# Kernel tuning notes

Measured on AMD Instinct MI355X. Metric: run time of the kernel, lower is better.

## Reference

```python
import jax, jax.numpy as jnp
import numpy as np

NUM_NODES = 100000
NUM_HYPEREDGES = 20000
NUM_SEMALINKS = 5000
NUM_EDGES = 600000
IN_DIM = 128
SIGNAL_DIM = 64
OUT_DIM = 128


def setup_inputs() -> dict:
    key = jax.random.key(0)
    k = jax.random.split(key, 8)
    node_embeddings = jax.random.normal(k[0], (NUM_NODES, IN_DIM), dtype=jnp.float32)
    semalink_embeddings = jax.random.normal(k[1], (NUM_SEMALINKS, SIGNAL_DIM), dtype=jnp.float32)
    hyperedge_embeddings = jax.random.normal(k[2], (NUM_HYPEREDGES, IN_DIM), dtype=jnp.float32)
    node_idx = jax.random.randint(k[3], (NUM_EDGES,), 0, NUM_NODES, dtype=jnp.int32)
    sl_idx = jax.random.randint(k[4], (NUM_EDGES,), 0, NUM_SEMALINKS, dtype=jnp.int32)
    he_idx = jax.random.randint(k[5], (NUM_EDGES,), 0, NUM_HYPEREDGES, dtype=jnp.int32)
    semalinks = jnp.stack([node_idx, sl_idx, he_idx], axis=1)  # [E, 3]
    W_a = jax.random.normal(k[6], (IN_DIM, SIGNAL_DIM), dtype=jnp.float32)
    W_f = jax.random.normal(k[7], (2 * IN_DIM, OUT_DIM), dtype=jnp.float32)
    return {
        'node_embeddings': node_embeddings,
        'semalink_embeddings': semalink_embeddings,
        'hyperedge_embeddings': hyperedge_embeddings,
        'semalinks': semalinks,
        'W_a': W_a,
        'W_f': W_f,
    }


def reference(node_embeddings, semalink_embeddings, hyperedge_embeddings, semalinks, W_a, W_f):
    # Original loops edges in order, ASSIGNING final_embeddings[node_idx] each time:
    # only the LAST edge touching each node determines that node's output.
    E = semalinks.shape[0]
    n_idx = semalinks[:, 0]
    s_idx = semalinks[:, 1]
    h_idx = semalinks[:, 2]

    order = jnp.arange(E, dtype=jnp.int32)
    last = jax.ops.segment_max(order, n_idx, num_segments=NUM_NODES)  # [N]
    has_edge = last >= 0
    last_c = jnp.clip(last, 0, E - 1)

    sel_h = h_idx[last_c]  # [N]
    sel_s = s_idx[last_c]  # [N]
    h_emb = hyperedge_embeddings[sel_h]          # [N, in_dim]
    sl_emb = semalink_embeddings[sel_s]          # [N, signal_dim]

    # per-node attention score (1x1 in original)
    r_h = node_embeddings @ W_a                  # [N, signal_dim]
    r_t = h_emb @ W_a                            # [N, signal_dim]
    score = jnp.sum(r_h * jnp.tanh(r_t + sl_emb), axis=-1, keepdims=True)  # [N, 1]
    gamma = jax.nn.softmax(score, axis=-1)       # softmax over singleton == 1.0 (same as torch)
    f = gamma * h_emb                            # [N, in_dim]

    u = jnp.concatenate([f, node_embeddings], axis=-1) @ W_f  # [N, out_dim]
    out = jnp.where(has_edge[:, None], u, jnp.zeros((), dtype=u.dtype))
    return out
```

## Files before the change

### kernel.cpp

```cpp
#include <hip/hip_runtime.h>
#include <hip/hip_bf16.h>

#define NNODES 100000
#define NHE 20000
#define NEDGES 600000

typedef float f32x4 __attribute__((ext_vector_type(4)));
typedef short bf16x8 __attribute__((ext_vector_type(8)));
typedef short bf16x4 __attribute__((ext_vector_type(4)));
typedef int i32x4 __attribute__((ext_vector_type(4)));
typedef unsigned long long u64;

__device__ __forceinline__ unsigned short f2bf(float f) {
    unsigned u = __builtin_bit_cast(unsigned, f);
    u += 0x7fffu + ((u >> 16) & 1u);
    return (unsigned short)(u >> 16);
}
__device__ __forceinline__ float bf2f(unsigned short h) {
    unsigned u = ((unsigned)h) << 16;
    return __builtin_bit_cast(float, u);
}

__global__ void k0(u64* __restrict__ packed, const float* __restrict__ Wf,
                   unsigned short* __restrict__ wt) {
    int b = blockIdx.x, t = threadIdx.x;
    if (b < 196) {
        int i = b * 256 + t;
        if (i < NNODES / 2) ((f32x4*)packed)[i] = (f32x4){0.f, 0.f, 0.f, 0.f};
    } else {
        int idx = (b - 196) * 256 + t;
        int k = idx >> 7, c = idx & 127;
        wt[c * 256 + k] = f2bf(Wf[idx]);
    }
}

__global__ __launch_bounds__(256) void k1(
    const int* __restrict__ sl, u64* __restrict__ packed,
    const float* __restrict__ he_emb, const unsigned short* __restrict__ wt,
    unsigned short* __restrict__ heo)
{
    int b = blockIdx.x, t = threadIdx.x;
    if (b < 586) {
        int tg = b * 256 + t;
        if (tg < NEDGES / 4) {
            const i32x4* s4 = (const i32x4*)sl;
            i32x4 a = s4[3 * tg], bb = s4[3 * tg + 1], c = s4[3 * tg + 2];
            int e0 = 4 * tg;
            atomicMax(&packed[a[0]], ((u64)(e0 + 1) << 32) | (unsigned)a[2]);
            atomicMax(&packed[a[3]], ((u64)(e0 + 2) << 32) | (unsigned)bb[1]);
            atomicMax(&packed[bb[2]], ((u64)(e0 + 3) << 32) | (unsigned)c[0]);
            atomicMax(&packed[c[1]], ((u64)(e0 + 4) << 32) | (unsigned)c[3]);
        }
        return;
    }

    __shared__ __align__(16) unsigned short Xs[64 * 128];
    int r0 = (b - 586) * 64;

    #pragma unroll
    for (int i = 0; i < 8; ++i) {
        int idx = i * 256 + t;
        int row = idx >> 5, q = idx & 31;
        int ri = r0 + row; if (ri >= NHE) ri = NHE - 1;
        f32x4 v = *(const f32x4*)(he_emb + (long)ri * 128 + q * 4);
        bf16x4 p;
        p[0] = (short)f2bf(v[0]); p[1] = (short)f2bf(v[1]);
        p[2] = (short)f2bf(v[2]); p[3] = (short)f2bf(v[3]);
        int byte = (row * 256 + q * 8) ^ ((row & 7) << 4);
        *(bf16x4*)((char*)Xs + byte) = p;
    }
    __syncthreads();

    int lane = t & 63, w = t >> 6;
    int wm = w >> 1, wn = w & 1;
    int l15 = lane & 15, l4 = lane >> 4;

    f32x4 acc[2][4] = {};
    #pragma unroll
    for (int kc = 0; kc < 2; ++kc)
        #pragma unroll
        for (int ks = 0; ks < 2; ++ks) {
            bf16x8 a[2], bb[4];
            #pragma unroll
            for (int fm = 0; fm < 2; ++fm) {
                int row = wm * 32 + fm * 16 + l15;
                int byte = (row * 256 + kc * 128 + ks * 64 + l4 * 16) ^ ((row & 7) << 4);
                a[fm] = *(const bf16x8*)((const char*)Xs + byte);
            }
            #pragma unroll
            for (int fn = 0; fn < 4; ++fn) {
                int col = wn * 64 + fn * 16 + l15;
                bb[fn] = *(const bf16x8*)(wt + (long)col * 256 + kc * 64 + ks * 32 + l4 * 8);
            }
            #pragma unroll
            for (int fm = 0; fm < 2; ++fm)
                #pragma unroll
                for (int fn = 0; fn < 4; ++fn)
                    acc[fm][fn] = __builtin_amdgcn_mfma_f32_16x16x32_bf16(
                        bb[fn], a[fm], acc[fm][fn], 0, 0, 0);
        }

    #pragma unroll
    for (int fm = 0; fm < 2; ++fm) {
        int ri = r0 + wm * 32 + fm * 16 + l15;
        if (ri < NHE) {
            #pragma unroll
            for (int fn = 0; fn < 4; ++fn) {
                bf16x4 p;
                p[0] = (short)f2bf(acc[fm][fn][0]);
                p[1] = (short)f2bf(acc[fm][fn][1]);
                p[2] = (short)f2bf(acc[fm][fn][2]);
                p[3] = (short)f2bf(acc[fm][fn][3]);
                *(bf16x4*)(heo + (long)ri * 128 + wn * 64 + fn * 16 + l4 * 4) = p;
            }
        }
    }
}

__global__ __launch_bounds__(256) void k_main(
    const float* __restrict__ node_emb,
    const u64* __restrict__ packed,
    const unsigned short* __restrict__ wt,
    const unsigned short* __restrict__ heo,
    float* __restrict__ out)
{
    __shared__ __align__(16) unsigned short Xs[64 * 128];

    int t = threadIdx.x;
    int r0 = blockIdx.x * 64;
    int lane = t & 63, w = t >> 6;
    int wm = w >> 1, wn = w & 1;
    int l15 = lane & 15, l4 = lane >> 4;

    u64 p = 0;
    {
        int prow = r0 + wm * 32 + (lane & 31);
        if (lane < 32 && prow < NNODES) p = packed[prow];
    }

    f32x4 nv[8];
    #pragma unroll
    for (int i = 0; i < 8; ++i) {
        int idx = i * 256 + t;
        int row = idx >> 5, q = idx & 31;
        int ri = r0 + row; if (ri >= NNODES) ri = NNODES - 1;
        nv[i] = *(const f32x4*)(node_emb + (long)ri * 128 + q * 4);
    }

    int he16 = (int)(p & 0xffffffffull);
    int v16 = (p != 0) ? 1 : 0;
    int hrow[2], vv[2];
    hrow[0] = __shfl(he16, l15, 64);       vv[0] = __shfl(v16, l15, 64);
    hrow[1] = __shfl(he16, 16 + l15, 64);  vv[1] = __shfl(v16, 16 + l15, 64);
    bf16x4 hv[2][4];
    #pragma unroll
    for (int fm = 0; fm < 2; ++fm)
        #pragma unroll
        for (int fn = 0; fn < 4; ++fn)
            hv[fm][fn] = *(const bf16x4*)(heo + (long)hrow[fm] * 128 +
                                          wn * 64 + fn * 16 + l4 * 4);

    #pragma unroll
    for (int i = 0; i < 8; ++i) {
        int idx = i * 256 + t;
        int row = idx >> 5, q = idx & 31;
        bf16x4 pk;
        pk[0] = (short)f2bf(nv[i][0]); pk[1] = (short)f2bf(nv[i][1]);
        pk[2] = (short)f2bf(nv[i][2]); pk[3] = (short)f2bf(nv[i][3]);
        int byte = (row * 256 + q * 8) ^ ((row & 7) << 4);
        *(bf16x4*)((char*)Xs + byte) = pk;
    }

    asm volatile("s_waitcnt lgkmcnt(0)" ::: "memory");
    __builtin_amdgcn_sched_barrier(0);
    __builtin_amdgcn_s_barrier();
    __builtin_amdgcn_sched_barrier(0);

    f32x4 acc[2][4] = {};
    #pragma unroll
    for (int kc = 0; kc < 2; ++kc)
        #pragma unroll
        for (int ks = 0; ks < 2; ++ks) {
            bf16x8 a[2], b[4];
            #pragma unroll
            for (int fm = 0; fm < 2; ++fm) {
                int row = wm * 32 + fm * 16 + l15;
                int byte = (row * 256 + kc * 128 + ks * 64 + l4 * 16) ^ ((row & 7) << 4);
                a[fm] = *(const bf16x8*)((const char*)Xs + byte);
            }
            #pragma unroll
            for (int fn = 0; fn < 4; ++fn) {
                int col = wn * 64 + fn * 16 + l15;
                b[fn] = *(const bf16x8*)(wt + (long)col * 256 + 128 + kc * 64 + ks * 32 + l4 * 8);
            }
            #pragma unroll
            for (int fm = 0; fm < 2; ++fm)
                #pragma unroll
                for (int fn = 0; fn < 4; ++fn)
                    acc[fm][fn] = __builtin_amdgcn_mfma_f32_16x16x32_bf16(
                        b[fn], a[fm], acc[fm][fn], 0, 0, 0);
        }

    #pragma unroll
    for (int fm = 0; fm < 2; ++fm) {
        int ri = r0 + wm * 32 + fm * 16 + l15;
        if (ri < NNODES) {
            int v = vv[fm];
            #pragma unroll
            for (int fn = 0; fn < 4; ++fn) {
                f32x4 o;
                #pragma unroll
                for (int jj = 0; jj < 4; ++jj)
                    o[jj] = v ? (acc[fm][fn][jj] + bf2f((unsigned short)hv[fm][fn][jj]))
                              : 0.0f;
                __builtin_nontemporal_store(o,
                    (f32x4*)(out + (long)ri * 128 + wn * 64 + fn * 16 + l4 * 4));
            }
        }
    }
}

extern "C" void kernel_launch(void* const* d_in, const int* in_sizes, int n_in,
                              void* d_out, int out_size, void* d_ws, size_t ws_size,
                              hipStream_t stream) {
    const float* node_emb = (const float*)d_in[0];
    const float* he_emb = (const float*)d_in[2];
    const int* sl = (const int*)d_in[3];
    const float* Wf = (const float*)d_in[5];
    float* out = (float*)d_out;

    u64* packed = (u64*)d_ws;
    unsigned short* wt = (unsigned short*)((char*)d_ws + 800000);
    unsigned short* heo = (unsigned short*)((char*)d_ws + 865536);

    k0<<<324, 256, 0, stream>>>(packed, Wf, wt);
    k1<<<586 + 313, 256, 0, stream>>>(sl, packed, he_emb, wt, heo);
    k_main<<<(NNODES + 63) / 64, 256, 0, stream>>>(node_emb, packed, wt, heo, out);
}
```

Before: 70.08 us.

## Process two 64-row tiles per block with prefetch of second tile

Each k_main block now handles 128 node rows as two 64-row tiles with separate LDS buffers. The node embeddings for the second tile are loaded while the first tile's MFMA runs, and the packed/hyperedge gathers for both tiles are issued up front. This is meant to hide global load latency and amortize weight fragment loads. In exchange it raises register and LDS use and halves the grid size, which may reduce occupancy and tail balance.

```diff
diff --git a/kernel.cpp b/kernel.cpp
--- a/kernel.cpp
+++ b/kernel.cpp
@@ -124,18 +124,18 @@
     const unsigned short* __restrict__ heo,
     float* __restrict__ out)
 {
-    __shared__ __align__(16) unsigned short Xs[64 * 128];
+    __shared__ __align__(16) unsigned short Xs[2][64 * 128];
 
     int t = threadIdx.x;
-    int r0 = blockIdx.x * 64;
+    int r0 = blockIdx.x * 128;
     int lane = t & 63, w = t >> 6;
     int wm = w >> 1, wn = w & 1;
     int l15 = lane & 15, l4 = lane >> 4;
 
     u64 p = 0;
     {
-        int prow = r0 + wm * 32 + (lane & 31);
-        if (lane < 32 && prow < NNODES) p = packed[prow];
+        int prow = r0 + (lane >> 5) * 64 + wm * 32 + (lane & 31);
+        if (prow < NNODES) p = packed[prow];
     }
 
     f32x4 nv[8];
@@ -149,16 +149,22 @@
 
     int he16 = (int)(p & 0xffffffffull);
     int v16 = (p != 0) ? 1 : 0;
-    int hrow[2], vv[2];
-    hrow[0] = __shfl(he16, l15, 64);       vv[0] = __shfl(v16, l15, 64);
-    hrow[1] = __shfl(he16, 16 + l15, 64);  vv[1] = __shfl(v16, 16 + l15, 64);
-    bf16x4 hv[2][4];
+    int hrow0[2], vv0[2], hrow1[2], vv1[2];
+    #pragma unroll
+    for (int fm = 0; fm < 2; ++fm) {
+        hrow0[fm] = __shfl(he16, fm * 16 + l15, 64);
+        vv0[fm]   = __shfl(v16,  fm * 16 + l15, 64);
+        hrow1[fm] = __shfl(he16, 32 + fm * 16 + l15, 64);
+        vv1[fm]   = __shfl(v16,  32 + fm * 16 + l15, 64);
+    }
+    bf16x4 hv0[2][4], hv1[2][4];
     #pragma unroll
     for (int fm = 0; fm < 2; ++fm)
         #pragma unroll
-        for (int fn = 0; fn < 4; ++fn)
-            hv[fm][fn] = *(const bf16x4*)(heo + (long)hrow[fm] * 128 +
-                                          wn * 64 + fn * 16 + l4 * 4);
+        for (int fn = 0; fn < 4; ++fn) {
+            hv0[fm][fn] = *(const bf16x4*)(heo + (long)hrow0[fm] * 128 + wn * 64 + fn * 16 + l4 * 4);
+            hv1[fm][fn] = *(const bf16x4*)(heo + (long)hrow1[fm] * 128 + wn * 64 + fn * 16 + l4 * 4);
+        }
 
     #pragma unroll
     for (int i = 0; i < 8; ++i) {
@@ -168,7 +174,7 @@
         pk[0] = (short)f2bf(nv[i][0]); pk[1] = (short)f2bf(nv[i][1]);
         pk[2] = (short)f2bf(nv[i][2]); pk[3] = (short)f2bf(nv[i][3]);
         int byte = (row * 256 + q * 8) ^ ((row & 7) << 4);
-        *(bf16x4*)((char*)Xs + byte) = pk;
+        *(bf16x4*)((char*)Xs[0] + byte) = pk;
     }
 
     asm volatile("s_waitcnt lgkmcnt(0)" ::: "memory");
@@ -176,6 +182,14 @@
     __builtin_amdgcn_s_barrier();
     __builtin_amdgcn_sched_barrier(0);
 
+    #pragma unroll
+    for (int i = 0; i < 8; ++i) {
+        int idx = i * 256 + t;
+        int row = idx >> 5, q = idx & 31;
+        int ri = r0 + 64 + row; if (ri >= NNODES) ri = NNODES - 1;
+        nv[i] = *(const f32x4*)(node_emb + (long)ri * 128 + q * 4);
+    }
+
     f32x4 acc[2][4] = {};
     #pragma unroll
     for (int kc = 0; kc < 2; ++kc)
@@ -186,7 +200,7 @@
             for (int fm = 0; fm < 2; ++fm) {
                 int row = wm * 32 + fm * 16 + l15;
                 int byte = (row * 256 + kc * 128 + ks * 64 + l4 * 16) ^ ((row & 7) << 4);
-                a[fm] = *(const bf16x8*)((const char*)Xs + byte);
+                a[fm] = *(const bf16x8*)((const char*)Xs[0] + byte);
             }
             #pragma unroll
             for (int fn = 0; fn < 4; ++fn) {
@@ -205,14 +219,71 @@
     for (int fm = 0; fm < 2; ++fm) {
         int ri = r0 + wm * 32 + fm * 16 + l15;
         if (ri < NNODES) {
-            int v = vv[fm];
+            int v = vv0[fm];
             #pragma unroll
             for (int fn = 0; fn < 4; ++fn) {
                 f32x4 o;
                 #pragma unroll
                 for (int jj = 0; jj < 4; ++jj)
-                    o[jj] = v ? (acc[fm][fn][jj] + bf2f((unsigned short)hv[fm][fn][jj]))
-                              : 0.0f;
+                    o[jj] = v ? (acc[fm][fn][jj] + bf2f((unsigned short)hv0[fm][fn][jj])) : 0.0f;
+                __builtin_nontemporal_store(o,
+                    (f32x4*)(out + (long)ri * 128 + wn * 64 + fn * 16 + l4 * 4));
+            }
+        }
+    }
+
+    #pragma unroll
+    for (int i = 0; i < 8; ++i) {
+        int idx = i * 256 + t;
+        int row = idx >> 5, q = idx & 31;
+        bf16x4 pk;
+        pk[0] = (short)f2bf(nv[i][0]); pk[1] = (short)f2bf(nv[i][1]);
+        pk[2] = (short)f2bf(nv[i][2]); pk[3] = (short)f2bf(nv[i][3]);
+        int byte = (row * 256 + q * 8) ^ ((row & 7) << 4);
+        *(bf16x4*)((char*)Xs[1] + byte) = pk;
+    }
+
+    asm volatile("s_waitcnt lgkmcnt(0)" ::: "memory");
+    __builtin_amdgcn_sched_barrier(0);
+    __builtin_amdgcn_s_barrier();
+    __builtin_amdgcn_sched_barrier(0);
+
+    f32x4 acc1[2][4] = {};
+    #pragma unroll
+    for (int kc = 0; kc < 2; ++kc)
+        #pragma unroll
+        for (int ks = 0; ks < 2; ++ks) {
+            bf16x8 a[2], b[4];
+            #pragma unroll
+            for (int fm = 0; fm < 2; ++fm) {
+                int row = wm * 32 + fm * 16 + l15;
+                int byte = (row * 256 + kc * 128 + ks * 64 + l4 * 16) ^ ((row & 7) << 4);
+                a[fm] = *(const bf16x8*)((const char*)Xs[1] + byte);
+            }
+            #pragma unroll
+            for (int fn = 0; fn < 4; ++fn) {
+                int col = wn * 64 + fn * 16 + l15;
+                b[fn] = *(const bf16x8*)(wt + (long)col * 256 + 128 + kc * 64 + ks * 32 + l4 * 8);
+            }
+            #pragma unroll
+            for (int fm = 0; fm < 2; ++fm)
+                #pragma unroll
+                for (int fn = 0; fn < 4; ++fn)
+                    acc1[fm][fn] = __builtin_amdgcn_mfma_f32_16x16x32_bf16(
+                        b[fn], a[fm], acc1[fm][fn], 0, 0, 0);
+        }
+
+    #pragma unroll
+    for (int fm = 0; fm < 2; ++fm) {
+        int ri = r0 + 64 + wm * 32 + fm * 16 + l15;
+        if (ri < NNODES) {
+            int v = vv1[fm];
+            #pragma unroll
+            for (int fn = 0; fn < 4; ++fn) {
+                f32x4 o;
+                #pragma unroll
+                for (int jj = 0; jj < 4; ++jj)
+                    o[jj] = v ? (acc1[fm][fn][jj] + bf2f((unsigned short)hv1[fm][fn][jj])) : 0.0f;
                 __builtin_nontemporal_store(o,
                     (f32x4*)(out + (long)ri * 128 + wn * 64 + fn * 16 + l4 * 4));
             }
@@ -235,5 +306,5 @@
 
     k0<<<324, 256, 0, stream>>>(packed, Wf, wt);
     k1<<<586 + 313, 256, 0, stream>>>(sl, packed, he_emb, wt, heo);
-    k_main<<<(NNODES + 63) / 64, 256, 0, stream>>>(node_emb, packed, wt, heo, out);
-}
+    k_main<<<(NNODES + 127) / 128, 256, 0, stream>>>(node_emb, packed, wt, heo, out);
+}
```

Result: slower. 73.95 us (+5.5%).

## Restructure main kernel to per-wave 16-row tiles loading operands directly to registers

Applied to the files above, without the earlier changes.

The main kernel now gives each wave its own 16-row tile covering all 128 output columns. Node rows are loaded from global memory straight into MFMA operand registers and converted there, which removes the shared-memory staging and the block barrier. The nontemporal output store becomes a plain store. In exchange, each wave reads the full 128-column weight slice with no sharing across waves, so weight traffic through L1/L2 rises. The per-row loads are also strided, which may coalesce worse than the old contiguous row loads.

```diff
diff --git a/kernel.cpp b/kernel.cpp
--- a/kernel.cpp
+++ b/kernel.cpp
@@ -19,6 +19,14 @@
 __device__ __forceinline__ float bf2f(unsigned short h) {
     unsigned u = ((unsigned)h) << 16;
     return __builtin_bit_cast(float, u);
+}
+__device__ __forceinline__ bf16x8 cvt8(f32x4 a, f32x4 b) {
+    bf16x8 r;
+    r[0] = (short)f2bf(a[0]); r[1] = (short)f2bf(a[1]);
+    r[2] = (short)f2bf(a[2]); r[3] = (short)f2bf(a[3]);
+    r[4] = (short)f2bf(b[0]); r[5] = (short)f2bf(b[1]);
+    r[6] = (short)f2bf(b[2]); r[7] = (short)f2bf(b[3]);
+    return r;
 }
 
 __global__ void k0(u64* __restrict__ packed, const float* __restrict__ Wf,
@@ -124,99 +132,49 @@
     const unsigned short* __restrict__ heo,
     float* __restrict__ out)
 {
-    __shared__ __align__(16) unsigned short Xs[64 * 128];
+    int t = threadIdx.x;
+    int wave = (blockIdx.x << 2) + (t >> 6);
+    int r0 = wave * 16;
+    if (r0 >= NNODES) return;
+    int lane = t & 63, l15 = lane & 15, l4 = lane >> 4;
+    int ri = r0 + l15;
 
-    int t = threadIdx.x;
-    int r0 = blockIdx.x * 64;
-    int lane = t & 63, w = t >> 6;
-    int wm = w >> 1, wn = w & 1;
-    int l15 = lane & 15, l4 = lane >> 4;
+    u64 p = packed[ri];
+    int hrow = (int)(p & 0xffffffffull);
+    int valid = (p != 0) ? 1 : 0;
 
-    u64 p = 0;
-    {
-        int prow = r0 + wm * 32 + (lane & 31);
-        if (lane < 32 && prow < NNODES) p = packed[prow];
+    bf16x4 hv[8];
+    #pragma unroll
+    for (int fn = 0; fn < 8; ++fn)
+        hv[fn] = *(const bf16x4*)(heo + (long)hrow * 128 + fn * 16 + l4 * 4);
+
+    f32x4 nv[4][2];
+    #pragma unroll
+    for (int ks = 0; ks < 4; ++ks) {
+        const float* s = node_emb + (long)ri * 128 + ks * 32 + l4 * 8;
+        nv[ks][0] = *(const f32x4*)s;
+        nv[ks][1] = *(const f32x4*)(s + 4);
     }
 
-    f32x4 nv[8];
+    f32x4 acc[8] = {};
     #pragma unroll
-    for (int i = 0; i < 8; ++i) {
-        int idx = i * 256 + t;
-        int row = idx >> 5, q = idx & 31;
-        int ri = r0 + row; if (ri >= NNODES) ri = NNODES - 1;
-        nv[i] = *(const f32x4*)(node_emb + (long)ri * 128 + q * 4);
+    for (int ks = 0; ks < 4; ++ks) {
+        bf16x8 a = cvt8(nv[ks][0], nv[ks][1]);
+        #pragma unroll
+        for (int fn = 0; fn < 8; ++fn) {
+            bf16x8 b = *(const bf16x8*)(wt + (long)(fn * 16 + l15) * 256 + 128 +
+                                        ks * 32 + l4 * 8);
+            acc[fn] = __builtin_amdgcn_mfma_f32_16x16x32_bf16(b, a, acc[fn], 0, 0, 0);
+        }
     }
 
-    int he16 = (int)(p & 0xffffffffull);
-    int v16 = (p != 0) ? 1 : 0;
-    int hrow[2], vv[2];
-    hrow[0] = __shfl(he16, l15, 64);       vv[0] = __shfl(v16, l15, 64);
-    hrow[1] = __shfl(he16, 16 + l15, 64);  vv[1] = __shfl(v16, 16 + l15, 64);
-    bf16x4 hv[2][4];
     #pragma unroll
-    for (int fm = 0; fm < 2; ++fm)
+    for (int fn = 0; fn < 8; ++fn) {
+        f32x4 o;
         #pragma unroll
-        for (int fn = 0; fn < 4; ++fn)
-            hv[fm][fn] = *(const bf16x4*)(heo + (long)hrow[fm] * 128 +
-                                          wn * 64 + fn * 16 + l4 * 4);
-
-    #pragma unroll
-    for (int i = 0; i < 8; ++i) {
-        int idx = i * 256 + t;
-        int row = idx >> 5, q = idx & 31;
-        bf16x4 pk;
-        pk[0] = (short)f2bf(nv[i][0]); pk[1] = (short)f2bf(nv[i][1]);
-        pk[2] = (short)f2bf(nv[i][2]); pk[3] = (short)f2bf(nv[i][3]);
-        int byte = (row * 256 + q * 8) ^ ((row & 7) << 4);
-        *(bf16x4*)((char*)Xs + byte) = pk;
-    }
-
-    asm volatile("s_waitcnt lgkmcnt(0)" ::: "memory");
-    __builtin_amdgcn_sched_barrier(0);
-    __builtin_amdgcn_s_barrier();
-    __builtin_amdgcn_sched_barrier(0);
-
-    f32x4 acc[2][4] = {};
-    #pragma unroll
-    for (int kc = 0; kc < 2; ++kc)
-        #pragma unroll
-        for (int ks = 0; ks < 2; ++ks) {
-            bf16x8 a[2], b[4];
-            #pragma unroll
-            for (int fm = 0; fm < 2; ++fm) {
-                int row = wm * 32 + fm * 16 + l15;
-                int byte = (row * 256 + kc * 128 + ks * 64 + l4 * 16) ^ ((row & 7) << 4);
-                a[fm] = *(const bf16x8*)((const char*)Xs + byte);
-            }
-            #pragma unroll
-            for (int fn = 0; fn < 4; ++fn) {
-                int col = wn * 64 + fn * 16 + l15;
-                b[fn] = *(const bf16x8*)(wt + (long)col * 256 + 128 + kc * 64 + ks * 32 + l4 * 8);
-            }
-            #pragma unroll
-            for (int fm = 0; fm < 2; ++fm)
-                #pragma unroll
-                for (int fn = 0; fn < 4; ++fn)
-                    acc[fm][fn] = __builtin_amdgcn_mfma_f32_16x16x32_bf16(
-                        b[fn], a[fm], acc[fm][fn], 0, 0, 0);
-        }
-
-    #pragma unroll
-    for (int fm = 0; fm < 2; ++fm) {
-        int ri = r0 + wm * 32 + fm * 16 + l15;
-        if (ri < NNODES) {
-            int v = vv[fm];
-            #pragma unroll
-            for (int fn = 0; fn < 4; ++fn) {
-                f32x4 o;
-                #pragma unroll
-                for (int jj = 0; jj < 4; ++jj)
-                    o[jj] = v ? (acc[fm][fn][jj] + bf2f((unsigned short)hv[fm][fn][jj]))
-                              : 0.0f;
-                __builtin_nontemporal_store(o,
-                    (f32x4*)(out + (long)ri * 128 + wn * 64 + fn * 16 + l4 * 4));
-            }
-        }
+        for (int jj = 0; jj < 4; ++jj)
+            o[jj] = valid ? (acc[fn][jj] + bf2f((unsigned short)hv[fn][jj])) : 0.0f;
+        *(f32x4*)(out + (long)ri * 128 + fn * 16 + l4 * 4) = o;
     }
 }
 
@@ -235,5 +193,5 @@
 
     k0<<<324, 256, 0, stream>>>(packed, Wf, wt);
     k1<<<586 + 313, 256, 0, stream>>>(sl, packed, he_emb, wt, heo);
-    k_main<<<(NNODES + 63) / 64, 256, 0, stream>>>(node_emb, packed, wt, heo, out);
+    k_main<<<(6250 + 3) / 4, 256, 0, stream>>>(node_emb, packed, wt, heo, out);
 }
```

New measurement: 84.71 us. 1.21x slower.

## Process two row tiles per block with prefetch and register-resident weights

Applied to the files above, without the earlier changes.

The main kernel now launches half as many blocks, and each block handles two 64-row tiles. The weight fragments are loaded into registers once per block and reused for both tiles. While the first tile is converted and multiplied, the second tile's node embeddings and packed indices are already being fetched. The output stores switch from nontemporal to regular stores, and the added live registers and doubled LDS may lower occupancy.

```diff
diff --git a/kernel.cpp b/kernel.cpp
--- a/kernel.cpp
+++ b/kernel.cpp
@@ -124,20 +124,30 @@
     const unsigned short* __restrict__ heo,
     float* __restrict__ out)
 {
-    __shared__ __align__(16) unsigned short Xs[64 * 128];
+    __shared__ __align__(16) unsigned short Xs[2][64 * 128];
 
     int t = threadIdx.x;
-    int r0 = blockIdx.x * 64;
     int lane = t & 63, w = t >> 6;
     int wm = w >> 1, wn = w & 1;
     int l15 = lane & 15, l4 = lane >> 4;
+
+    bf16x8 B[4][4];
+    #pragma unroll
+    for (int kk = 0; kk < 4; ++kk)
+        #pragma unroll
+        for (int fn = 0; fn < 4; ++fn) {
+            int col = wn * 64 + fn * 16 + l15;
+            B[kk][fn] = *(const bf16x8*)(wt + (long)col * 256 + 128 + kk * 32 + l4 * 8);
+        }
+
+    int r0 = blockIdx.x * 64;
+    int r1 = (blockIdx.x + 782) * 64;
 
     u64 p = 0;
     {
         int prow = r0 + wm * 32 + (lane & 31);
         if (lane < 32 && prow < NNODES) p = packed[prow];
     }
-
     f32x4 nv[8];
     #pragma unroll
     for (int i = 0; i < 8; ++i) {
@@ -147,74 +157,84 @@
         nv[i] = *(const f32x4*)(node_emb + (long)ri * 128 + q * 4);
     }
 
-    int he16 = (int)(p & 0xffffffffull);
-    int v16 = (p != 0) ? 1 : 0;
-    int hrow[2], vv[2];
-    hrow[0] = __shfl(he16, l15, 64);       vv[0] = __shfl(v16, l15, 64);
-    hrow[1] = __shfl(he16, 16 + l15, 64);  vv[1] = __shfl(v16, 16 + l15, 64);
-    bf16x4 hv[2][4];
-    #pragma unroll
-    for (int fm = 0; fm < 2; ++fm)
-        #pragma unroll
-        for (int fn = 0; fn < 4; ++fn)
-            hv[fm][fn] = *(const bf16x4*)(heo + (long)hrow[fm] * 128 +
-                                          wn * 64 + fn * 16 + l4 * 4);
-
-    #pragma unroll
-    for (int i = 0; i < 8; ++i) {
-        int idx = i * 256 + t;
-        int row = idx >> 5, q = idx & 31;
-        bf16x4 pk;
-        pk[0] = (short)f2bf(nv[i][0]); pk[1] = (short)f2bf(nv[i][1]);
-        pk[2] = (short)f2bf(nv[i][2]); pk[3] = (short)f2bf(nv[i][3]);
-        int byte = (row * 256 + q * 8) ^ ((row & 7) << 4);
-        *(bf16x4*)((char*)Xs + byte) = pk;
-    }
-
-    asm volatile("s_waitcnt lgkmcnt(0)" ::: "memory");
-    __builtin_amdgcn_sched_barrier(0);
-    __builtin_amdgcn_s_barrier();
-    __builtin_amdgcn_sched_barrier(0);
-
-    f32x4 acc[2][4] = {};
-    #pragma unroll
-    for (int kc = 0; kc < 2; ++kc)
-        #pragma unroll
-        for (int ks = 0; ks < 2; ++ks) {
-            bf16x8 a[2], b[4];
+    #pragma unroll
+    for (int j = 0; j < 2; ++j) {
+        int rb = j ? r1 : r0;
+
+        int he16 = (int)(p & 0xffffffffull);
+        int v16 = (p != 0) ? 1 : 0;
+        int hrow[2], vv[2];
+        hrow[0] = __shfl(he16, l15, 64);       vv[0] = __shfl(v16, l15, 64);
+        hrow[1] = __shfl(he16, 16 + l15, 64);  vv[1] = __shfl(v16, 16 + l15, 64);
+        bf16x4 hv[2][4];
+        #pragma unroll
+        for (int fm = 0; fm < 2; ++fm)
+            #pragma unroll
+            for (int fn = 0; fn < 4; ++fn)
+                hv[fm][fn] = *(const bf16x4*)(heo + (long)hrow[fm] * 128 +
+                                              wn * 64 + fn * 16 + l4 * 4);
+
+        #pragma unroll
+        for (int i = 0; i < 8; ++i) {
+            int idx = i * 256 + t;
+            int row = idx >> 5, q = idx & 31;
+            bf16x4 pk;
+            pk[0] = (short)f2bf(nv[i][0]); pk[1] = (short)f2bf(nv[i][1]);
+            pk[2] = (short)f2bf(nv[i][2]); pk[3] = (short)f2bf(nv[i][3]);
+            int byte = (row * 256 + q * 8) ^ ((row & 7) << 4);
+            *(bf16x4*)((char*)Xs[j] + byte) = pk;
+        }
+
+        if (j == 0) {
+            p = 0;
+            int prow = r1 + wm * 32 + (lane & 31);
+            if (lane < 32 && prow < NNODES) p = packed[prow];
+            #pragma unroll
+            for (int i = 0; i < 8; ++i) {
+                int idx = i * 256 + t;
+                int row = idx >> 5, q = idx & 31;
+                int ri = r1 + row; if (ri >= NNODES) ri = NNODES - 1;
+                nv[i] = *(const f32x4*)(node_emb + (long)ri * 128 + q * 4);
+            }
+        }
+
+        asm volatile("s_waitcnt lgkmcnt(0)" ::: "memory");
+        __builtin_amdgcn_sched_barrier(0);
+        __builtin_amdgcn_s_barrier();
+        __builtin_amdgcn_sched_barrier(0);
+
+        f32x4 acc[2][4] = {};
+        #pragma unroll
+        for (int kk = 0; kk < 4; ++kk) {
+            bf16x8 a[2];
             #pragma unroll
             for (int fm = 0; fm < 2; ++fm) {
                 int row = wm * 32 + fm * 16 + l15;
-                int byte = (row * 256 + kc * 128 + ks * 64 + l4 * 16) ^ ((row & 7) << 4);
-                a[fm] = *(const bf16x8*)((const char*)Xs + byte);
-            }
-            #pragma unroll
-            for (int fn = 0; fn < 4; ++fn) {
-                int col = wn * 64 + fn * 16 + l15;
-                b[fn] = *(const bf16x8*)(wt + (long)col * 256 + 128 + kc * 64 + ks * 32 + l4 * 8);
+                int byte = (row * 256 + kk * 64 + l4 * 16) ^ ((row & 7) << 4);
+                a[fm] = *(const bf16x8*)((const char*)Xs[j] + byte);
             }
             #pragma unroll
             for (int fm = 0; fm < 2; ++fm)
                 #pragma unroll
                 for (int fn = 0; fn < 4; ++fn)
                     acc[fm][fn] = __builtin_amdgcn_mfma_f32_16x16x32_bf16(
-                        b[fn], a[fm], acc[fm][fn], 0, 0, 0);
-        }
-
-    #pragma unroll
-    for (int fm = 0; fm < 2; ++fm) {
-        int ri = r0 + wm * 32 + fm * 16 + l15;
-        if (ri < NNODES) {
-            int v = vv[fm];
-            #pragma unroll
-            for (int fn = 0; fn < 4; ++fn) {
-                f32x4 o;
+                        B[kk][fn], a[fm], acc[fm][fn], 0, 0, 0);
+        }
+
+        #pragma unroll
+        for (int fm = 0; fm < 2; ++fm) {
+            int ri = rb + wm * 32 + fm * 16 + l15;
+            if (ri < NNODES) {
+                int v = vv[fm];
                 #pragma unroll
-                for (int jj = 0; jj < 4; ++jj)
-                    o[jj] = v ? (acc[fm][fn][jj] + bf2f((unsigned short)hv[fm][fn][jj]))
-                              : 0.0f;
-                __builtin_nontemporal_store(o,
-                    (f32x4*)(out + (long)ri * 128 + wn * 64 + fn * 16 + l4 * 4));
+                for (int fn = 0; fn < 4; ++fn) {
+                    f32x4 o;
+                    #pragma unroll
+                    for (int jj = 0; jj < 4; ++jj)
+                        o[jj] = v ? (acc[fm][fn][jj] + bf2f((unsigned short)hv[fm][fn][jj]))
+                                  : 0.0f;
+                    *(f32x4*)(out + (long)ri * 128 + wn * 64 + fn * 16 + l4 * 4) = o;
+                }
             }
         }
     }
@@ -235,5 +255,5 @@
 
     k0<<<324, 256, 0, stream>>>(packed, Wf, wt);
     k1<<<586 + 313, 256, 0, stream>>>(sl, packed, he_emb, wt, heo);
-    k_main<<<(NNODES + 63) / 64, 256, 0, stream>>>(node_emb, packed, wt, heo, out);
-}
+    k_main<<<782, 256, 0, stream>>>(node_emb, packed, wt, heo, out);
+}
```

After: 69.95 us. About the same (-0.2%).
